# Optimization experiments

Hardware: AMD Instinct MI355X
Metric: run time of the kernel (lower is better)

## Reference

```python
import jax, jax.numpy as jnp
import numpy as np

R = 16
LORA_ALPHA = 16
SCALING = LORA_ALPHA / R  # 1.0


def setup_inputs() -> dict:
    key = jax.random.key(0)
    kx, kr, ka = jax.random.split(key, 3)
    B, S, D, DO, E = 4, 2048, 4096, 4096, 8
    x = jax.random.normal(kx, (B, S, D), dtype=jnp.float32)
    # kaiming_uniform_(a=sqrt(5)) on Linear weight of fan_in=D -> U(-1/sqrt(D), 1/sqrt(D))
    bound_r = 1.0 / np.sqrt(D)
    route_w = jax.random.uniform(kr, (E, D), jnp.float32, -bound_r, bound_r)  # lora_route.weight
    bound_a = 1.0 / np.sqrt(D)
    A = jax.random.uniform(ka, (E, R, D), jnp.float32, -bound_a, bound_a)  # stacked lora_A{i}.weight [r, D]
    # lora_B weights are zero-initialized in the module; use small random for a nontrivial baseline
    kb = jax.random.fold_in(key, 7)
    Bw = jax.random.normal(kb, (E, DO, R), dtype=jnp.float32) * 0.02  # stacked lora_B{i}.weight [DO, r]
    return {"x": x, "route_w": route_w, "A": A, "Bw": Bw}


def reference(x, route_w, A, Bw):
    # router logits [B, S, E]
    logits = jnp.einsum("bsd,ed->bse", x, route_w)
    # top-1 hard routing: keep raw logit value at the argmax slot, zero elsewhere
    topk_v, topk_idx = jax.lax.top_k(logits, 1)  # [B,S,1]
    E = logits.shape[-1]
    route_weight = jax.nn.one_hot(topk_idx[..., 0], E, dtype=logits.dtype) * topk_v  # [B,S,E]
    # low-rank per-expert projections (dense over experts, as in the original loop)
    h = jnp.einsum("bsd,erd->bser", x, A)            # [B,S,E,r]
    wh = route_weight[..., None] * h                  # weight before the up-projection
    out = jnp.einsum("bser,eor->bso", wh, Bw) * SCALING  # [B,S,DO]
    return out
```

## Files before the change

kernel.cpp:

```cpp
#include <hip/hip_runtime.h>
#include <hip/hip_bf16.h>

#define DD   4096
#define NE   8
#define NR   16
#define NTOK 8192
#define NDO  4096
#define TAU  0.01f
#define MAXFLAG 8000

typedef __attribute__((ext_vector_type(8))) __bf16 bf16x8;
typedef __attribute__((ext_vector_type(4))) __bf16 bf16x4;
typedef __attribute__((ext_vector_type(4))) float  f32x4;

__device__ __forceinline__ bf16x8 to_bf16x8(float4 a, float4 b) {
    bf16x8 r;
    r[0] = (__bf16)a.x; r[1] = (__bf16)a.y; r[2] = (__bf16)a.z; r[3] = (__bf16)a.w;
    r[4] = (__bf16)b.x; r[5] = (__bf16)b.y; r[6] = (__bf16)b.z; r[7] = (__bf16)b.w;
    return r;
}

__device__ __forceinline__ bf16x8 zero_frag() {
    bf16x8 z;
    #pragma unroll
    for (int j = 0; j < 8; j++) z[j] = (__bf16)0.0f;
    return z;
}

__global__ __launch_bounds__(256) void k_prep_w(const float* __restrict__ rw,
                                                const float* __restrict__ Am,
                                                const float* __restrict__ Bw,
                                                __bf16* __restrict__ rwhl,
                                                __bf16* __restrict__ Ab,
                                                __bf16* __restrict__ Bwb) {
    const int b = blockIdx.x;
    if (b < 1024) {
        const int o = (b & 511) * 1024 + threadIdx.x * 4;
        const float4 v = *(const float4*)(((b < 512) ? Bw : Am) + o);
        bf16x4 p;
        p[0] = (__bf16)v.x; p[1] = (__bf16)v.y; p[2] = (__bf16)v.z; p[3] = (__bf16)v.w;
        *(bf16x4*)(((b < 512) ? Bwb : Ab) + o) = p;
    } else {
        const int o = (b - 1024) * 1024 + threadIdx.x * 4;
        const int row = o >> 12, k = o & 4095;
        const float4 v = *(const float4*)(rw + ((size_t)(row & 7) << 12) + k);
        bf16x4 p;
        if (row < 8) {
            p[0] = (__bf16)v.x; p[1] = (__bf16)v.y; p[2] = (__bf16)v.z; p[3] = (__bf16)v.w;
        } else {
            p[0] = (__bf16)(v.x - (float)(__bf16)v.x);
            p[1] = (__bf16)(v.y - (float)(__bf16)v.y);
            p[2] = (__bf16)(v.z - (float)(__bf16)v.z);
            p[3] = (__bf16)(v.w - (float)(__bf16)v.w);
        }
        *(bf16x4*)(rwhl + o) = p;
    }
}

__global__ __launch_bounds__(256, 1) void k_route_part(const float* __restrict__ x,
                                                       const __bf16* __restrict__ rwhl,
                                                       float* __restrict__ pbuf) {
    const int tg = blockIdx.x >> 2;
    const int kg = blockIdx.x & 3;
    const int t0 = tg * 16;
    const int wv = threadIdx.x >> 6;
    const int lane = threadIdx.x & 63;
    const int m = lane & 15;
    const int half = lane >> 4;

    const float*  xrow = x    + (size_t)(t0 + m) * DD;
    const __bf16* wrow = rwhl + (size_t)m * DD;

    f32x4 acc = {0.f, 0.f, 0.f, 0.f};
    const int kbase = kg * 1024 + wv * 256;
    #pragma unroll
    for (int ks = 0; ks < 8; ks++) {
        const int k0 = kbase + ks * 32 + half * 8;
        const float4 xa = *(const float4*)(xrow + k0);
        const float4 xc = *(const float4*)(xrow + k0 + 4);
        const bf16x8 wb = *(const bf16x8*)(wrow + k0);
        acc = __builtin_amdgcn_mfma_f32_16x16x32_bf16(to_bf16x8(xa, xc), wb, acc, 0, 0, 0);
    }

    __shared__ float Lred[4][16][17];
    #pragma unroll
    for (int r = 0; r < 4; r++)
        Lred[wv][half * 4 + r][m] = acc[r];
    __syncthreads();

    if (threadIdx.x < 128) {
        const int t = threadIdx.x >> 3, ee = threadIdx.x & 7;
        float s = 0.f;
        #pragma unroll
        for (int w = 0; w < 4; w++) s += Lred[w][t][ee] + Lred[w][t][ee + 8];
        pbuf[((size_t)kg * NTOK + t0 + t) * NE + ee] = s;
    }
}

__global__ __launch_bounds__(256) void k_route_fin(const float* __restrict__ pbuf,
                                                   float* __restrict__ w_arr,
                                                   int*   __restrict__ token_list,
                                                   int*   __restrict__ count,
                                                   int*   __restrict__ nflag,
                                                   int*   __restrict__ flaglist) {
    const int tok = blockIdx.x * 256 + threadIdx.x;
    float l[NE];
    #pragma unroll
    for (int e = 0; e < NE; e++)
        l[e] = pbuf[((size_t)0 * NTOK + tok) * NE + e]
             + pbuf[((size_t)1 * NTOK + tok) * NE + e]
             + pbuf[((size_t)2 * NTOK + tok) * NE + e]
             + pbuf[((size_t)3 * NTOK + tok) * NE + e];

    float best = -1e30f, second = -1e30f; int be = 0;
    #pragma unroll
    for (int e = 0; e < NE; e++) {
        if (l[e] > best) { second = best; best = l[e]; be = e; }
        else if (l[e] > second) { second = l[e]; }
    }
    w_arr[tok] = best;
    if (best - second < TAU) {
        const int p = atomicAdd(nflag, 1);
        if (p < MAXFLAG) flaglist[p] = tok;
    } else {
        const int p = atomicAdd(&count[be], 1);
        token_list[be * NTOK + p] = tok;
    }
}

__global__ __launch_bounds__(256) void k_fix(const float* __restrict__ x,
                                             const float* __restrict__ rw,
                                             float* __restrict__ w_arr,
                                             int*   __restrict__ token_list,
                                             int*   __restrict__ count,
                                             const int* __restrict__ nflag,
                                             const int* __restrict__ flaglist) {
    const int wv   = threadIdx.x >> 6;
    const int lane = threadIdx.x & 63;
    int n = *nflag; if (n > MAXFLAG) n = MAXFLAG;

    for (int idx = blockIdx.x * 4 + wv; idx < n; idx += 512) {
        const int tok = flaglist[idx];
        const float* xp = x + (size_t)tok * DD;
        double acc[NE];
        #pragma unroll
        for (int e = 0; e < NE; e++) acc[e] = 0.0;
        for (int i = 0; i < 16; i++) {
            const int d4 = (i * 64 + lane) * 4;
            const float4 xv = *(const float4*)(xp + d4);
            const double x0 = xv.x, x1 = xv.y, x2 = xv.z, x3 = xv.w;
            #pragma unroll
            for (int e = 0; e < NE; e++) {
                const float4 wv4 = *(const float4*)(rw + (size_t)e * DD + d4);
                acc[e] = fma(x0, (double)wv4.x, acc[e]);
                acc[e] = fma(x1, (double)wv4.y, acc[e]);
                acc[e] = fma(x2, (double)wv4.z, acc[e]);
                acc[e] = fma(x3, (double)wv4.w, acc[e]);
            }
        }
        #pragma unroll
        for (int off = 32; off > 0; off >>= 1)
            #pragma unroll
            for (int e = 0; e < NE; e++)
                acc[e] += __shfl_xor(acc[e], off, 64);
        if (lane == 0) {
            double best = acc[0]; int be = 0;
            #pragma unroll
            for (int e = 1; e < NE; e++) if (acc[e] > best) { best = acc[e]; be = e; }
            w_arr[tok] = (float)best;
            const int pos = atomicAdd(&count[be], 1);
            token_list[be * NTOK + pos] = tok;
        }
    }
}

__global__ __launch_bounds__(1024) void k_h(const float* __restrict__ x,
                                            const __bf16* __restrict__ Ab,
                                            const float* __restrict__ w_arr,
                                            const int*   __restrict__ token_list,
                                            const int*   __restrict__ count,
                                            __hip_bfloat16* __restrict__ wh) {
    const int e    = blockIdx.x >> 7;
    const int g    = blockIdx.x & 127;
    const int cnt  = count[e];
    const int base = g * 32;
    if (base >= cnt) return;

    const int wv   = threadIdx.x >> 6;
    const int lane = threadIdx.x & 63;
    const int m    = lane & 15;
    const int half = lane >> 4;

    const int i0 = base + m,  i1 = base + 16 + m;
    const int tok0 = (i0 < cnt) ? token_list[e * NTOK + i0] : 0;
    const int tok1 = (i1 < cnt) ? token_list[e * NTOK + i1] : 0;
    const float*  xr0  = x  + (size_t)tok0 * DD;
    const float*  xr1  = x  + (size_t)tok1 * DD;
    const __bf16* arow = Ab + ((size_t)e * NR + m) * DD;

    f32x4 acc0 = {0.f,0.f,0.f,0.f}, acc1 = {0.f,0.f,0.f,0.f};
    const int kbase = wv * 256;
    #pragma unroll
    for (int kc = 0; kc < 8; kc++) {
        const int k0 = kbase + kc * 32 + half * 8;
        const bf16x8 bfrag = *(const bf16x8*)(arow + k0);
        const bf16x8 a0 = to_bf16x8(*(const float4*)(xr0 + k0),
                                    *(const float4*)(xr0 + k0 + 4));
        const bf16x8 a1 = to_bf16x8(*(const float4*)(xr1 + k0),
                                    *(const float4*)(xr1 + k0 + 4));
        acc0 = __builtin_amdgcn_mfma_f32_16x16x32_bf16(a0, bfrag, acc0, 0, 0, 0);
        acc1 = __builtin_amdgcn_mfma_f32_16x16x32_bf16(a1, bfrag, acc1, 0, 0, 0);
    }

    __shared__ float lds[16][32][17];
    #pragma unroll
    for (int rr = 0; rr < 4; rr++) {
        lds[wv][half * 4 + rr][m]      = acc0[rr];
        lds[wv][16 + half * 4 + rr][m] = acc1[rr];
    }
    __syncthreads();

    if (threadIdx.x < 512) {
        const int t = threadIdx.x >> 4;
        const int r = threadIdx.x & 15;
        const int i2 = base + t;
        if (i2 < cnt) {
            float s = 0.f;
            #pragma unroll
            for (int w = 0; w < 16; w++) s += lds[w][t][r];
            const int tk = token_list[e * NTOK + i2];
            wh[(size_t)tk * NR + r] = (__hip_bfloat16)(s * w_arr[tk]);
        }
    }
}

__global__ __launch_bounds__(256, 1) void k_out(const __bf16* __restrict__ Bwb,
                                                const __hip_bfloat16* __restrict__ wh,
                                                const int*   __restrict__ token_list,
                                                const int*   __restrict__ count,
                                                float* __restrict__ out) {
    const int bx    = blockIdx.x;
    const int chunk = bx & 3;
    const int slot  = (bx >> 2) & 511;
    const int e     = bx >> 11;
    const int cnt   = count[e];
    const int base  = slot * 16;
    if (base >= cnt) return;

    const int wv   = threadIdx.x >> 6;
    const int lane = threadIdx.x & 63;
    const int m    = lane & 15;
    const int half = lane >> 4;

    const int  idx   = base + m;
    const bool valid = idx < cnt;
    const int  tok   = valid ? token_list[e * NTOK + idx] : 0;
    const bf16x8 zf  = zero_frag();

    const bf16x8 a2 = (half < 2 && valid)
        ? *(const bf16x8*)((const __bf16*)wh + (size_t)tok * NR + half * 8)
        : zf;

    __shared__ float lds[16][1028];
    const __bf16* bwe = Bwb + (size_t)e * NDO * NR;
    const int h2 = (half < 2) ? half : 0;
    const f32x4 zero4 = {0.f, 0.f, 0.f, 0.f};
    const int ob0 = wv * 256;

    for (int g = 0; g < 2; g++) {
        bf16x8 B[8];
        #pragma unroll
        for (int i = 0; i < 8; i++) {
            const int oc = chunk * 1024 + ob0 + (g * 8 + i) * 16;
            B[i] = (half < 2)
                ? *(const bf16x8*)(bwe + (size_t)(oc + m) * NR + h2 * 8)
                : zf;
        }
        #pragma unroll
        for (int i = 0; i < 8; i++) {
            const f32x4 d = __builtin_amdgcn_mfma_f32_16x16x32_bf16(a2, B[i], zero4, 0, 0, 0);
            const int col = ob0 + (g * 8 + i) * 16 + m;
            #pragma unroll
            for (int r = 0; r < 4; r++)
                lds[half * 4 + r][col] = d[r];
        }
    }
    __syncthreads();

    #pragma unroll 4
    for (int r = 0; r < 16; r++) {
        const int ir = base + r;
        if (ir < cnt) {
            const int tr = token_list[e * NTOK + ir];
            const float4 v = *(const float4*)&lds[r][threadIdx.x * 4];
            float* dst = out + (size_t)tr * NDO + chunk * 1024 + threadIdx.x * 4;
            __builtin_nontemporal_store(v.x, dst + 0);
            __builtin_nontemporal_store(v.y, dst + 1);
            __builtin_nontemporal_store(v.z, dst + 2);
            __builtin_nontemporal_store(v.w, dst + 3);
        }
    }
}

extern "C" void kernel_launch(void* const* d_in, const int* in_sizes, int n_in,
                              void* d_out, int out_size, void* d_ws, size_t ws_size,
                              hipStream_t stream) {
    const float* x  = (const float*)d_in[0];
    const float* rw = (const float*)d_in[1];
    const float* Am = (const float*)d_in[2];
    const float* Bw = (const float*)d_in[3];
    float* out = (float*)d_out;

    char* ws = (char*)d_ws;
    int*   count      = (int*)ws;
    int*   nflag      = (int*)(ws + 32);
    float* w_arr      = (float*)(ws + 512);
    int*   flaglist   = (int*)(ws + 33280);
    int*   token_list = (int*)(ws + 65536);
    __hip_bfloat16* wh = (__hip_bfloat16*)(ws + 327680);
    __bf16* rwhl      = (__bf16*)(ws + 589824);
    __bf16* Bwb       = (__bf16*)(ws + 720896);
    __bf16* Ab        = (__bf16*)(ws + 1769472);
    float*  pbuf      = (float*)(ws + 3145728);

    hipMemsetAsync(ws, 0, 64, stream);
    hipLaunchKernelGGL(k_prep_w,     dim3(1088),  dim3(256), 0, stream, rw, Am, Bw, rwhl, Ab, Bwb);
    hipLaunchKernelGGL(k_route_part, dim3(2048),  dim3(256), 0, stream, x, rwhl, pbuf);
    hipLaunchKernelGGL(k_route_fin,  dim3(32),    dim3(256), 0, stream, pbuf, w_arr, token_list, count, nflag, flaglist);
    hipLaunchKernelGGL(k_fix,        dim3(128),   dim3(256), 0, stream, x, rw, w_arr, token_list, count, nflag, flaglist);
    hipLaunchKernelGGL(k_h,          dim3(1024),  dim3(1024),0, stream, x, Ab, w_arr, token_list, count, wh);
    hipLaunchKernelGGL(k_out,        dim3(16384), dim3(256), 0, stream, Bwb, wh, token_list, count, out);
}
```

Before: 149.2 us.

## Store k_out MFMA results directly to global, skipping the LDS staging

The output kernel is restructured. Each block now handles 64 tokens × 512 output columns instead of 16 tokens × 1024 columns. The MFMA operands are swapped so each lane's f32x4 result lies along the output dimension of one token, which lets it be written straight to global memory with a nontemporal 16-byte store. The LDS staging buffer and the barrier go away, the next B fragment is prefetched in software, and the single-block occupancy limit is dropped. The cost is narrower per-lane stores (16 bytes at a stride of one row per token) and fewer blocks per expert.

```diff
diff --git a/kernel.cpp b/kernel.cpp
--- a/kernel.cpp
+++ b/kernel.cpp
@@ -234,70 +234,59 @@
     }
 }
 
-__global__ __launch_bounds__(256, 1) void k_out(const __bf16* __restrict__ Bwb,
-                                                const __hip_bfloat16* __restrict__ wh,
-                                                const int*   __restrict__ token_list,
-                                                const int*   __restrict__ count,
-                                                float* __restrict__ out) {
+__global__ __launch_bounds__(256) void k_out(const __bf16* __restrict__ Bwb,
+                                             const __hip_bfloat16* __restrict__ wh,
+                                             const int*   __restrict__ token_list,
+                                             const int*   __restrict__ count,
+                                             float* __restrict__ out) {
     const int bx    = blockIdx.x;
-    const int chunk = bx & 3;
-    const int slot  = (bx >> 2) & 511;
-    const int e     = bx >> 11;
+    const int e     = bx >> 10;
+    const int slot  = (bx >> 3) & 127;
+    const int chunk = bx & 7;
     const int cnt   = count[e];
-    const int base  = slot * 16;
+    const int base  = slot * 64;
     if (base >= cnt) return;
 
     const int wv   = threadIdx.x >> 6;
     const int lane = threadIdx.x & 63;
     const int m    = lane & 15;
     const int half = lane >> 4;
-
-    const int  idx   = base + m;
-    const bool valid = idx < cnt;
-    const int  tok   = valid ? token_list[e * NTOK + idx] : 0;
-    const bf16x8 zf  = zero_frag();
-
-    const bf16x8 a2 = (half < 2 && valid)
-        ? *(const bf16x8*)((const __bf16*)wh + (size_t)tok * NR + half * 8)
+    const int h2   = (half < 2) ? half : 0;
+    const bf16x8 zf = zero_frag();
+
+    bf16x8 a2[4]; int trow[4]; bool vst[4];
+    #pragma unroll
+    for (int s = 0; s < 4; s++) {
+        const int idx = base + s * 16 + m;
+        vst[s]  = idx < cnt;
+        trow[s] = vst[s] ? token_list[e * NTOK + idx] : 0;
+        a2[s] = (half < 2 && vst[s])
+            ? *(const bf16x8*)((const __bf16*)wh + (size_t)trow[s] * NR + half * 8)
+            : zf;
+    }
+
+    const __bf16* bwe = Bwb + (size_t)e * NDO * NR;
+    const int ot0 = chunk * 32 + wv * 8;
+    const f32x4 zero4 = {0.f, 0.f, 0.f, 0.f};
+
+    bf16x8 bq = (half < 2)
+        ? *(const bf16x8*)(bwe + (size_t)(ot0 * 16 + m) * NR + h2 * 8)
         : zf;
-
-    __shared__ float lds[16][1028];
-    const __bf16* bwe = Bwb + (size_t)e * NDO * NR;
-    const int h2 = (half < 2) ? half : 0;
-    const f32x4 zero4 = {0.f, 0.f, 0.f, 0.f};
-    const int ob0 = wv * 256;
-
-    for (int g = 0; g < 2; g++) {
-        bf16x8 B[8];
+    #pragma unroll
+    for (int i = 0; i < 8; i++) {
+        const bf16x8 b2 = bq;
+        if (i < 7) {
+            bq = (half < 2)
+                ? *(const bf16x8*)(bwe + (size_t)((ot0 + i + 1) * 16 + m) * NR + h2 * 8)
+                : zf;
+        }
+        const int ob = (ot0 + i) * 16;
         #pragma unroll
-        for (int i = 0; i < 8; i++) {
-            const int oc = chunk * 1024 + ob0 + (g * 8 + i) * 16;
-            B[i] = (half < 2)
-                ? *(const bf16x8*)(bwe + (size_t)(oc + m) * NR + h2 * 8)
-                : zf;
-        }
-        #pragma unroll
-        for (int i = 0; i < 8; i++) {
-            const f32x4 d = __builtin_amdgcn_mfma_f32_16x16x32_bf16(a2, B[i], zero4, 0, 0, 0);
-            const int col = ob0 + (g * 8 + i) * 16 + m;
-            #pragma unroll
-            for (int r = 0; r < 4; r++)
-                lds[half * 4 + r][col] = d[r];
-        }
-    }
-    __syncthreads();
-
-    #pragma unroll 4
-    for (int r = 0; r < 16; r++) {
-        const int ir = base + r;
-        if (ir < cnt) {
-            const int tr = token_list[e * NTOK + ir];
-            const float4 v = *(const float4*)&lds[r][threadIdx.x * 4];
-            float* dst = out + (size_t)tr * NDO + chunk * 1024 + threadIdx.x * 4;
-            __builtin_nontemporal_store(v.x, dst + 0);
-            __builtin_nontemporal_store(v.y, dst + 1);
-            __builtin_nontemporal_store(v.z, dst + 2);
-            __builtin_nontemporal_store(v.w, dst + 3);
+        for (int s = 0; s < 4; s++) {
+            const f32x4 d = __builtin_amdgcn_mfma_f32_16x16x32_bf16(b2, a2[s], zero4, 0, 0, 0);
+            if (vst[s])
+                __builtin_nontemporal_store(d,
+                    (f32x4*)(out + (size_t)trow[s] * NDO + ob + half * 4));
         }
     }
 }
@@ -329,5 +318,5 @@
     hipLaunchKernelGGL(k_route_fin,  dim3(32),    dim3(256), 0, stream, pbuf, w_arr, token_list, count, nflag, flaglist);
     hipLaunchKernelGGL(k_fix,        dim3(128),   dim3(256), 0, stream, x, rw, w_arr, token_list, count, nflag, flaglist);
     hipLaunchKernelGGL(k_h,          dim3(1024),  dim3(1024),0, stream, x, Ab, w_arr, token_list, count, wh);
-    hipLaunchKernelGGL(k_out,        dim3(16384), dim3(256), 0, stream, Bwb, wh, token_list, count, out);
-}
+    hipLaunchKernelGGL(k_out,        dim3(8192),  dim3(256), 0, stream, Bwb, wh, token_list, count, out);
+}
```

Result: slower. 172.0 us (+15.3%).
